# Performance work log

Measured on AMD Instinct MI355X. Metric: run time of the kernel, lower is better.

Reference implementation:

```python
import jax, jax.numpy as jnp
import numpy as np

# Module config (from init_kwargs): levels = [8]*6, channels = 64
LEVELS = (8, 8, 8, 8, 8, 8)
# basis = cumprod([1] + levels[:-1])
BASIS = np.cumprod([1] + list(LEVELS[:-1])).astype(np.int32)  # [1,8,64,512,4096,32768]


def setup_inputs() -> dict:
    key = jax.random.key(0)
    k_z, k_p, k_c = jax.random.split(key, 3)
    B, N = 2_000_000, len(LEVELS)
    max_level = max(LEVELS)
    channels = 64
    codebook_size = int(np.prod(LEVELS))  # 262144
    z = jax.random.normal(k_z, (B, N), dtype=jnp.float32)
    # percentiles: sorted per-dimension bin edges (mimics torch.quantile output)
    percentiles = jnp.sort(jax.random.normal(k_p, (max_level, N), dtype=jnp.float32), axis=0)
    codebook = jax.random.normal(k_c, (codebook_size, channels), dtype=jnp.float32)
    return {"z": z, "percentiles": percentiles, "codebook": codebook}


def reference(z, percentiles, codebook):
    # quantize: sequential overwrite indices[mask]=j for j=0..num_bins-1 with
    # mask = z[:, i] >= percentiles[j, i]  ->  final index = max{ j : z >= p[j] }, else 0.
    J = percentiles.shape[0]  # max_level (all levels equal here)
    cond = z[:, None, :] >= percentiles[None, :, :]              # [B, J, N] bool
    j_ids = jnp.arange(J, dtype=jnp.int32)[None, :, None]        # [1, J, 1]
    indices = jnp.max(jnp.where(cond, j_ids, 0), axis=1)         # [B, N] int32
    big_index = jnp.sum(indices * jnp.asarray(BASIS)[None, :], axis=-1)  # [B]
    quantized = codebook[big_index]                              # [B, channels] gather
    return quantized, big_index
```

## Files before the change

### kernel.cpp

```cpp
#include <hip/hip_runtime.h>


#define NDIM 6
#define NLEV 8
#define CH 64
#define ROWS_PER_BLOCK 64
#define THREADS 256

__global__ __launch_bounds__(THREADS) void fsq_kernel(
    const float* __restrict__ z,
    const float* __restrict__ perc,
    const float* __restrict__ codebook,
    float* __restrict__ out_q,
    float* __restrict__ out_idx,
    int B)
{
    __shared__ float s_z[ROWS_PER_BLOCK * NDIM];
    __shared__ float s_p[NLEV * NDIM];
    __shared__ int   s_idx[ROWS_PER_BLOCK];

    const int tid = threadIdx.x;
    const long long row0 = (long long)blockIdx.x * ROWS_PER_BLOCK;

    if (tid < NLEV * NDIM) s_p[tid] = perc[tid];

    int nrows = ROWS_PER_BLOCK;
    if (row0 + ROWS_PER_BLOCK > (long long)B) nrows = (int)((long long)B - row0);
    const int nz = nrows * NDIM;
    const float* zbase = z + row0 * NDIM;
    for (int i = tid; i < nz; i += THREADS) s_z[i] = zbase[i];
    __syncthreads();

    if (tid < nrows) {
        const int basis[NDIM] = {1, 8, 64, 512, 4096, 32768};
        int big = 0;
        #pragma unroll
        for (int d = 0; d < NDIM; ++d) {
            const float zv = s_z[tid * NDIM + d];
            int cnt = 0;
            #pragma unroll
            for (int j = 0; j < NLEV; ++j)
                cnt += (zv >= s_p[j * NDIM + d]) ? 1 : 0;
            const int idx = (cnt > 0) ? (cnt - 1) : 0;
            big += idx * basis[d];
        }
        s_idx[tid] = big;
        out_idx[row0 + tid] = (float)big;
    }
    __syncthreads();

    const int lane = tid & 15;
    const int rsub = tid >> 4;
    for (int r = rsub; r < nrows; r += 16) {
        const long long big = (long long)s_idx[r];
        const float4* __restrict__ src =
            (const float4*)(codebook + big * CH);
        float4* __restrict__ dst =
            (float4*)(out_q + (row0 + r) * (long long)CH);
        dst[lane] = src[lane];
    }
}

extern "C" void kernel_launch(void* const* d_in, const int* in_sizes, int n_in,
                              void* d_out, int out_size, void* d_ws, size_t ws_size,
                              hipStream_t stream) {
    const float* z        = (const float*)d_in[0];
    const float* perc     = (const float*)d_in[1];
    const float* codebook = (const float*)d_in[2];

    const int B = in_sizes[0] / NDIM;

    float* out_q   = (float*)d_out;
    float* out_idx = (float*)d_out + (long long)B * CH;

    const int grid = (B + ROWS_PER_BLOCK - 1) / ROWS_PER_BLOCK;
    fsq_kernel<<<grid, THREADS, 0, stream>>>(z, perc, codebook, out_q, out_idx, B);
}
```

Measured before the change: 626.9 us.

## Process more rows per block with vector loads, nontemporal stores, fused index-and-gather

Each block now handles 256 rows instead of 64. Full blocks load z with vectorized nontemporal loads. The separate index pass, its shared-memory index buffer and the second barrier are removed: each 16-lane group computes the index redundantly and then gathers its codebook row directly. Output rows are written with nontemporal stores, and the basis multiply is replaced by shifts. This cuts launch and barrier overhead and cache pollution from streaming writes, at the cost of redundant index computation across 16 lanes and fewer blocks.

```diff
diff --git a/kernel.cpp b/kernel.cpp
--- a/kernel.cpp
+++ b/kernel.cpp
@@ -4,8 +4,10 @@
 #define NDIM 6
 #define NLEV 8
 #define CH 64
-#define ROWS_PER_BLOCK 64
+#define ROWS 256
 #define THREADS 256
+
+typedef float f32x4 __attribute__((ext_vector_type(4)));
 
 __global__ __launch_bounds__(THREADS) void fsq_kernel(
     const float* __restrict__ z,
@@ -15,49 +17,59 @@
     float* __restrict__ out_idx,
     int B)
 {
-    __shared__ float s_z[ROWS_PER_BLOCK * NDIM];
+    __shared__ float s_z[ROWS * NDIM];
     __shared__ float s_p[NLEV * NDIM];
-    __shared__ int   s_idx[ROWS_PER_BLOCK];
 
     const int tid = threadIdx.x;
-    const long long row0 = (long long)blockIdx.x * ROWS_PER_BLOCK;
+    const long long row0 = (long long)blockIdx.x * ROWS;
 
     if (tid < NLEV * NDIM) s_p[tid] = perc[tid];
 
-    int nrows = ROWS_PER_BLOCK;
-    if (row0 + ROWS_PER_BLOCK > (long long)B) nrows = (int)((long long)B - row0);
-    const int nz = nrows * NDIM;
-    const float* zbase = z + row0 * NDIM;
-    for (int i = tid; i < nz; i += THREADS) s_z[i] = zbase[i];
+    int nrows = ROWS;
+    if (row0 + ROWS > (long long)B) nrows = (int)((long long)B - row0);
+
+    if (nrows == ROWS) {
+        const f32x4* __restrict__ zb = (const f32x4*)(z + row0 * NDIM);
+        {
+            f32x4 v = __builtin_nontemporal_load(&zb[tid]);
+            ((f32x4*)s_z)[tid] = v;
+        }
+        if (tid < (ROWS * NDIM) / 4 - THREADS) {
+            const int idx = tid + THREADS;
+            f32x4 v = __builtin_nontemporal_load(&zb[idx]);
+            ((f32x4*)s_z)[idx] = v;
+        }
+    } else {
+        const float* __restrict__ zb = z + row0 * NDIM;
+        for (int i = tid; i < nrows * NDIM; i += THREADS)
+            s_z[i] = zb[i];
+    }
     __syncthreads();
 
-    if (tid < nrows) {
-        const int basis[NDIM] = {1, 8, 64, 512, 4096, 32768};
+    const int lane = tid & 15;
+    const int g    = tid >> 4;
+
+    #pragma unroll 4
+    for (int r = g; r < nrows; r += 16) {
         int big = 0;
         #pragma unroll
         for (int d = 0; d < NDIM; ++d) {
-            const float zv = s_z[tid * NDIM + d];
+            const float zv = s_z[r * NDIM + d];
             int cnt = 0;
             #pragma unroll
             for (int j = 0; j < NLEV; ++j)
                 cnt += (zv >= s_p[j * NDIM + d]) ? 1 : 0;
-            const int idx = (cnt > 0) ? (cnt - 1) : 0;
-            big += idx * basis[d];
+            int idx = cnt - 1;
+            if (idx < 0) idx = 0;
+            big |= idx << (3 * d);
         }
-        s_idx[tid] = big;
-        out_idx[row0 + tid] = (float)big;
-    }
-    __syncthreads();
 
-    const int lane = tid & 15;
-    const int rsub = tid >> 4;
-    for (int r = rsub; r < nrows; r += 16) {
-        const long long big = (long long)s_idx[r];
-        const float4* __restrict__ src =
-            (const float4*)(codebook + big * CH);
-        float4* __restrict__ dst =
-            (float4*)(out_q + (row0 + r) * (long long)CH);
-        dst[lane] = src[lane];
+        const f32x4* __restrict__ src = (const f32x4*)(codebook + (long long)big * CH);
+        f32x4 v = src[lane];
+        f32x4* __restrict__ dst = (f32x4*)(out_q + (row0 + r) * (long long)CH);
+        __builtin_nontemporal_store(v, &dst[lane]);
+
+        if (lane == 0) out_idx[row0 + r] = (float)big;
     }
 }
 
@@ -73,6 +85,6 @@
     float* out_q   = (float*)d_out;
     float* out_idx = (float*)d_out + (long long)B * CH;
 
-    const int grid = (B + ROWS_PER_BLOCK - 1) / ROWS_PER_BLOCK;
+    const int grid = (B + ROWS - 1) / ROWS;
     fsq_kernel<<<grid, THREADS, 0, stream>>>(z, perc, codebook, out_q, out_idx, B);
 }
```

Result: slower. 640.0 us (+2.1%).
